# Kernel optimization log

Measured on AMD Instinct MI355X. Metric: run time of the kernel, lower is better.

The kernel has to match this reference:

```python
import jax, jax.numpy as jnp
import numpy as np

TOKENS = 16384
INPUT_DIM = 2048
NUM_EXPERTS = 16
K = 2


def setup_inputs() -> dict:
    key = jax.random.key(0)
    kx, kn, kw, kb = jax.random.split(key, 4)
    x = jax.random.normal(kx, (TOKENS, INPUT_DIM), dtype=jnp.float32)
    noise = jax.random.normal(kn, (TOKENS, NUM_EXPERTS), dtype=jnp.float32)
    # nn.Linear params: weight [out, in], bias [out]; kaiming-uniform-ish init
    bound = 1.0 / np.sqrt(INPUT_DIM)
    W = jax.random.uniform(kw, (NUM_EXPERTS, INPUT_DIM), dtype=jnp.float32, minval=-bound, maxval=bound)
    b = jax.random.uniform(kb, (NUM_EXPERTS,), dtype=jnp.float32, minval=-bound, maxval=bound)
    return {"x": x, "noise": noise, "W": W, "b": b}


def reference(x, noise, W, b):
    # logits: [tokens, num_experts]
    logits = jnp.einsum("td,ed->te", x, W) + b
    noisy_logits = logits + noise * 0.1
    top_k_values, top_k_indices = jax.lax.top_k(noisy_logits, K)  # [tokens, K]
    weights = jax.nn.softmax(top_k_values, axis=-1)               # [tokens, K]
    # scatter weights back into dense [tokens, num_experts] (zeros elsewhere)
    one_hot = jax.nn.one_hot(top_k_indices, NUM_EXPERTS, dtype=logits.dtype)  # [tokens, K, E]
    sparse_weights = jnp.einsum("tke,tk->te", one_hot, weights)
    return sparse_weights
```

## Files before the change

### kernel.cpp

```cpp
#include <hip/hip_runtime.h>
#include <hip/hip_bf16.h>
#include <math.h>

#define TOKENS 16384
#define DIM    2048
#define NEXP   16
#define CHUNK  256
#define NCHUNK (DIM / CHUNK)
#define TPB    16
#define NWAVE  4

typedef float fvec4 __attribute__((ext_vector_type(4)));
typedef float f32_as1 __attribute__((address_space(1)));
typedef float f32_as3 __attribute__((address_space(3)));

__device__ __forceinline__ void async_row(const float* gp, float* lp) {
    __builtin_amdgcn_global_load_lds((const f32_as1*)(const void*)gp,
                                     (f32_as3*)(uintptr_t)lp, 16, 0, 0);
}

__global__ __launch_bounds__(256, 4) void gating_moe_kernel(
    const float* __restrict__ x,
    const float* __restrict__ noise,
    const float* __restrict__ W,
    const float* __restrict__ b,
    float* __restrict__ out)
{
    __shared__ __align__(16) fvec4 wbuf[2][NEXP][CHUNK / 4];

    const int tid  = threadIdx.x;
    const int lane = tid & 63;
    const int w    = tid >> 6;
    const int block_base = blockIdx.x * TPB;
    const int lane4 = lane * 4;

    float r[64];
#pragma unroll
    for (int v = 0; v < 64; ++v) r[v] = 0.0f;

    const float* xr0 = x + (size_t)(block_base + w * 4 + 0) * DIM + lane4;
    const float* xr1 = xr0 + DIM;
    const float* xr2 = xr1 + DIM;
    const float* xr3 = xr2 + DIM;

#pragma unroll
    for (int q = 0; q < 4; ++q) {
        const int e = w * 4 + q;
        async_row(W + (size_t)e * DIM + lane4, (float*)&wbuf[0][e][0]);
    }
    fvec4 xv0 = __builtin_nontemporal_load((const fvec4*)xr0);
    fvec4 xv1 = __builtin_nontemporal_load((const fvec4*)xr1);
    fvec4 xv2 = __builtin_nontemporal_load((const fvec4*)xr2);
    fvec4 xv3 = __builtin_nontemporal_load((const fvec4*)xr3);
    __syncthreads();

#pragma unroll
    for (int c = 0; c < NCHUNK; ++c) {
        const int cur = c & 1, nxt = cur ^ 1;
        fvec4 xn0, xn1, xn2, xn3;
        if (c + 1 < NCHUNK) {
#pragma unroll
            for (int q = 0; q < 4; ++q) {
                const int e = w * 4 + q;
                async_row(W + (size_t)e * DIM + (c + 1) * CHUNK + lane4,
                          (float*)&wbuf[nxt][e][0]);
            }
            const int off = (c + 1) * CHUNK;
            xn0 = __builtin_nontemporal_load((const fvec4*)(xr0 + off));
            xn1 = __builtin_nontemporal_load((const fvec4*)(xr1 + off));
            xn2 = __builtin_nontemporal_load((const fvec4*)(xr2 + off));
            xn3 = __builtin_nontemporal_load((const fvec4*)(xr3 + off));
        }

#pragma unroll
        for (int eb = 0; eb < NEXP; eb += 2) {
            fvec4 wa = wbuf[cur][eb + 0][lane];
            fvec4 wc = wbuf[cur][eb + 1][lane];
#define FMA4(acc, xv, wv) acc = fmaf((xv).x,(wv).x, fmaf((xv).y,(wv).y, \
                                fmaf((xv).z,(wv).z, fmaf((xv).w,(wv).w,(acc)))))
            FMA4(r[0  * 16 + eb],     xv0, wa);
            FMA4(r[1  * 16 + eb],     xv1, wa);
            FMA4(r[2  * 16 + eb],     xv2, wa);
            FMA4(r[3  * 16 + eb],     xv3, wa);
            FMA4(r[0  * 16 + eb + 1], xv0, wc);
            FMA4(r[1  * 16 + eb + 1], xv1, wc);
            FMA4(r[2  * 16 + eb + 1], xv2, wc);
            FMA4(r[3  * 16 + eb + 1], xv3, wc);
#undef FMA4
        }
        __syncthreads();
        if (c + 1 < NCHUNK) { xv0 = xn0; xv1 = xn1; xv2 = xn2; xv3 = xn3; }
    }

#pragma unroll
    for (int s = 0; s < 6; ++s) {
        const int dist = 1 << s;
        const bool bsel = (lane >> s) & 1;
        const int n = 64 >> (s + 1);
#pragma unroll
        for (int i = 0; i < n; ++i) {
            float keep = bsel ? r[2 * i + 1] : r[2 * i];
            float send = bsel ? r[2 * i]     : r[2 * i + 1];
            r[i] = keep + __shfl_xor(send, dist);
        }
    }

    const int e = lane & 15;
    const size_t obase = (size_t)block_base * NEXP + (size_t)w * 64;
    float nz    = noise[obase + lane];
    float noisy = r[0] + b[e] + 0.1f * nz;

    float v1 = noisy; int i1 = e;
    float v2 = -INFINITY; int i2 = 999;
#pragma unroll
    for (int s = 0; s < 4; ++s) {
        const int d = 1 << s;
        float ov1 = __shfl_xor(v1, d); int oi1 = __shfl_xor(i1, d);
        float ov2 = __shfl_xor(v2, d); int oi2 = __shfl_xor(i2, d);
        bool awin = (v1 > ov1) || (v1 == ov1 && i1 < oi1);
        float t1v = awin ? v1  : ov1;  int t1i = awin ? i1  : oi1;
        float lv  = awin ? ov1 : v1;   int li  = awin ? oi1 : i1;
        float cv  = awin ? v2  : ov2;  int ci  = awin ? i2  : oi2;
        bool bwin = (cv > lv) || (cv == lv && ci < li);
        v1 = t1v; i1 = t1i;
        v2 = bwin ? cv : lv; i2 = bwin ? ci : li;
    }

    float dd = __expf(v2 - v1);
    float w1 = 1.0f / (1.0f + dd);
    float w2 = dd * w1;

    float o = (e == i1) ? w1 : ((e == i2) ? w2 : 0.0f);
    out[obase + lane] = o;
}

extern "C" void kernel_launch(void* const* d_in, const int* in_sizes, int n_in,
                              void* d_out, int out_size, void* d_ws, size_t ws_size,
                              hipStream_t stream) {
    const float* x     = (const float*)d_in[0];
    const float* noise = (const float*)d_in[1];
    const float* W     = (const float*)d_in[2];
    const float* b     = (const float*)d_in[3];
    float* out = (float*)d_out;

    dim3 grid(TOKENS / TPB);
    dim3 block(NWAVE * 64);
    gating_moe_kernel<<<grid, block, 0, stream>>>(x, noise, W, b, out);
}
```

Measured before the change: 188.4 us.

## Load gate weights directly from global memory instead of LDS double-buffering

```diff
diff --git a/kernel.cpp b/kernel.cpp
--- a/kernel.cpp
+++ b/kernel.cpp
@@ -11,13 +11,6 @@
 #define NWAVE  4
 
 typedef float fvec4 __attribute__((ext_vector_type(4)));
-typedef float f32_as1 __attribute__((address_space(1)));
-typedef float f32_as3 __attribute__((address_space(3)));
-
-__device__ __forceinline__ void async_row(const float* gp, float* lp) {
-    __builtin_amdgcn_global_load_lds((const f32_as1*)(const void*)gp,
-                                     (f32_as3*)(uintptr_t)lp, 16, 0, 0);
-}
 
 __global__ __launch_bounds__(256, 4) void gating_moe_kernel(
     const float* __restrict__ x,
@@ -26,8 +19,6 @@
     const float* __restrict__ b,
     float* __restrict__ out)
 {
-    __shared__ __align__(16) fvec4 wbuf[2][NEXP][CHUNK / 4];
-
     const int tid  = threadIdx.x;
     const int lane = tid & 63;
     const int w    = tid >> 6;
@@ -42,29 +33,17 @@
     const float* xr1 = xr0 + DIM;
     const float* xr2 = xr1 + DIM;
     const float* xr3 = xr2 + DIM;
+    const float* wp  = W + lane4;
 
-#pragma unroll
-    for (int q = 0; q < 4; ++q) {
-        const int e = w * 4 + q;
-        async_row(W + (size_t)e * DIM + lane4, (float*)&wbuf[0][e][0]);
-    }
     fvec4 xv0 = __builtin_nontemporal_load((const fvec4*)xr0);
     fvec4 xv1 = __builtin_nontemporal_load((const fvec4*)xr1);
     fvec4 xv2 = __builtin_nontemporal_load((const fvec4*)xr2);
     fvec4 xv3 = __builtin_nontemporal_load((const fvec4*)xr3);
-    __syncthreads();
 
 #pragma unroll
     for (int c = 0; c < NCHUNK; ++c) {
-        const int cur = c & 1, nxt = cur ^ 1;
         fvec4 xn0, xn1, xn2, xn3;
         if (c + 1 < NCHUNK) {
-#pragma unroll
-            for (int q = 0; q < 4; ++q) {
-                const int e = w * 4 + q;
-                async_row(W + (size_t)e * DIM + (c + 1) * CHUNK + lane4,
-                          (float*)&wbuf[nxt][e][0]);
-            }
             const int off = (c + 1) * CHUNK;
             xn0 = __builtin_nontemporal_load((const fvec4*)(xr0 + off));
             xn1 = __builtin_nontemporal_load((const fvec4*)(xr1 + off));
@@ -72,23 +51,25 @@
             xn3 = __builtin_nontemporal_load((const fvec4*)(xr3 + off));
         }
 
+        const float* wc = wp + c * CHUNK;
 #pragma unroll
-        for (int eb = 0; eb < NEXP; eb += 2) {
-            fvec4 wa = wbuf[cur][eb + 0][lane];
-            fvec4 wc = wbuf[cur][eb + 1][lane];
+        for (int eb = 0; eb < NEXP; eb += 4) {
+            fvec4 wv0 = *(const fvec4*)(wc + (size_t)(eb + 0) * DIM);
+            fvec4 wv1 = *(const fvec4*)(wc + (size_t)(eb + 1) * DIM);
+            fvec4 wv2 = *(const fvec4*)(wc + (size_t)(eb + 2) * DIM);
+            fvec4 wv3 = *(const fvec4*)(wc + (size_t)(eb + 3) * DIM);
 #define FMA4(acc, xv, wv) acc = fmaf((xv).x,(wv).x, fmaf((xv).y,(wv).y, \
                                 fmaf((xv).z,(wv).z, fmaf((xv).w,(wv).w,(acc)))))
-            FMA4(r[0  * 16 + eb],     xv0, wa);
-            FMA4(r[1  * 16 + eb],     xv1, wa);
-            FMA4(r[2  * 16 + eb],     xv2, wa);
-            FMA4(r[3  * 16 + eb],     xv3, wa);
-            FMA4(r[0  * 16 + eb + 1], xv0, wc);
-            FMA4(r[1  * 16 + eb + 1], xv1, wc);
-            FMA4(r[2  * 16 + eb + 1], xv2, wc);
-            FMA4(r[3  * 16 + eb + 1], xv3, wc);
+            FMA4(r[0*16+eb+0], xv0, wv0); FMA4(r[1*16+eb+0], xv1, wv0);
+            FMA4(r[2*16+eb+0], xv2, wv0); FMA4(r[3*16+eb+0], xv3, wv0);
+            FMA4(r[0*16+eb+1], xv0, wv1); FMA4(r[1*16+eb+1], xv1, wv1);
+            FMA4(r[2*16+eb+1], xv2, wv1); FMA4(r[3*16+eb+1], xv3, wv1);
+            FMA4(r[0*16+eb+2], xv0, wv2); FMA4(r[1*16+eb+2], xv1, wv2);
+            FMA4(r[2*16+eb+2], xv2, wv2); FMA4(r[3*16+eb+2], xv3, wv2);
+            FMA4(r[0*16+eb+3], xv0, wv3); FMA4(r[1*16+eb+3], xv1, wv3);
+            FMA4(r[2*16+eb+3], xv2, wv3); FMA4(r[3*16+eb+3], xv3, wv3);
 #undef FMA4
         }
-        __syncthreads();
         if (c + 1 < NCHUNK) { xv0 = xn0; xv1 = xn1; xv2 = xn2; xv3 = xn3; }
     }
 
```

New measurement: 231.8 us. +23.0%, slower.
